# Kernel tuning notes

Measured on AMD Instinct MI355X. Metric: run time of the kernel, lower is better.

## Reference

```python
import jax, jax.numpy as jnp
import numpy as np

B, S, DM, H = 8, 512, 1024, 16
D = DM // H            # head_dim = 64
NFEAT = 4              # len(feature_types)
N_DIST = 2 * 512 - 1   # max_utt_num*2-1 = 1023
N_DISC = 16 + 1        # len(DISCOURSE_RELATIONS)+1
N_COOC = 5 + 1


def setup_inputs() -> dict:
    key = jax.random.key(0)
    ks = jax.random.split(key, 24)
    inp = {}
    inp["query"] = jax.random.normal(ks[0], (B, S, DM), jnp.float32)
    inp["key"] = jax.random.normal(ks[1], (B, S, DM), jnp.float32)
    inp["value"] = jax.random.normal(ks[2], (B, S, DM), jnp.float32)
    inp["distance_adj"] = jax.random.randint(ks[3], (B, S, S), 0, N_DIST).astype(jnp.int32)
    inp["speaker_adj"] = jax.random.uniform(ks[4], (B, S, S), jnp.float32)
    inp["discourse_adj"] = jax.random.randint(ks[5], (B, S, S), 0, N_DISC).astype(jnp.int32)
    inp["cooccurrence_adj"] = jax.random.randint(ks[6], (B, S, S), 0, N_COOC).astype(jnp.int32)
    inp["mask"] = jnp.ones((B, 1, 1, S), jnp.int32)
    w = lambda k, shape: jax.random.normal(k, shape, jnp.float32) * 0.02
    inp["Wq"] = w(ks[7], (DM, DM)); inp["bq"] = jnp.zeros((DM,), jnp.float32)
    inp["Wk"] = w(ks[8], (DM, DM)); inp["bk"] = jnp.zeros((DM,), jnp.float32)
    inp["Wv"] = w(ks[9], (DM, DM)); inp["bv"] = jnp.zeros((DM,), jnp.float32)
    inp["Wo"] = w(ks[10], (DM, DM)); inp["bo"] = jnp.zeros((DM,), jnp.float32)
    inp["dist_embed"] = w(ks[11], (N_DIST, 1))
    inp["disc_embed"] = w(ks[12], (N_DISC, 1)).at[0].set(0.0)  # padding_idx=0
    inp["cooc_embed"] = w(ks[13], (N_COOC, 1)).at[0].set(0.0)  # padding_idx=0
    inp["fcw"] = w(ks[14], (H, NFEAT))       # per-head 1x1 conv weights
    inp["fcb"] = jnp.zeros((H,), jnp.float32)
    inp["cw"] = w(ks[15], (2,))              # combine conv weights
    inp["cb"] = jnp.zeros((), jnp.float32)
    return inp


def reference(query, key, value, distance_adj, speaker_adj, discourse_adj,
              cooccurrence_adj, mask, Wq, bq, Wk, bk, Wv, bv, Wo, bo,
              dist_embed, disc_embed, cooc_embed, fcw, fcb, cw, cb):
    scale = jnp.asarray(D ** 0.5, query.dtype)
    # Linear projections, split heads -> [B, H, S, D]
    split = lambda x: x.reshape(B, S, H, D).transpose(0, 2, 1, 3)
    Q = split(query @ Wq.T + bq)
    K = split(key @ Wk.T + bk)
    V = split(value @ Wv.T + bv)
    energy = jnp.einsum('bhqd,bhkd->bhqk', Q, K) / scale  # [B,H,S,S]
    # Adjacency feature maps in feature_types order: distance, speaker, discourse, cooccurrence
    dist = dist_embed[distance_adj, 0]
    disc = disc_embed[discourse_adj, 0] * (discourse_adj != 0)
    cooc = cooc_embed[cooccurrence_adj, 0] * (cooccurrence_adj != 0)
    feature_map = jnp.stack([dist, speaker_adj, disc, cooc], axis=1)  # [B,4,S,S]
    # Per-head 1x1 conv over the 4 feature channels + relu
    feat = jax.nn.relu(jnp.einsum('hc,bcij->bhij', fcw, feature_map)
                       + fcb[None, :, None, None])       # [B,H,S,S]
    # Combine conv (1x1, 2 channels -> 1) + relu
    energy = jax.nn.relu(cw[0] * energy + cw[1] * feat + cb)
    energy = jnp.where(mask == 0, -jnp.inf, energy)
    attention = jax.nn.softmax(energy, axis=-1)           # [B,H,S,S]
    x = jnp.einsum('bhqk,bhkd->bhqd', attention, V)       # dropout p=0 (eval)
    x = x.transpose(0, 2, 1, 3).reshape(B, S, DM)
    x = x @ Wo.T + bo
    return x, attention
```

## Files before the change

### kernel.cpp

```cpp
#include <hip/hip_runtime.h>

using short8 = __attribute__((ext_vector_type(8))) short;
using f32x4  = __attribute__((ext_vector_type(4))) float;

__device__ __forceinline__ unsigned short f2bf(float x) {
    union { float f; unsigned u; } v; v.f = x;
    unsigned u = v.u;
    unsigned r = (u + 0x7fffu + ((u >> 16) & 1u)) >> 16;
    return (unsigned short)r;
}
__device__ __forceinline__ float bf2f(unsigned short h) {
    union { unsigned u; float f; } v; v.u = ((unsigned)h) << 16;
    return v.f;
}

__device__ __forceinline__ void async16(const void* g, void* l) {
    __builtin_amdgcn_global_load_lds(
        (const __attribute__((address_space(1))) void*)g,
        (__attribute__((address_space(3))) void*)l, 16, 0, 0);
}

__global__ __launch_bounds__(256) void cvt_qkv(
    const float* __restrict__ q, const float* __restrict__ k, const float* __restrict__ v,
    unsigned short* __restrict__ dst)
{
    int z = blockIdx.z;
    const float* src = (z == 0) ? q : ((z == 1) ? k : v);
    unsigned short* o = dst + (size_t)z * 4194304;
    size_t i = ((size_t)blockIdx.x * 256 + threadIdx.x) * 8;
    float4 a = *(const float4*)(src + i);
    float4 b = *(const float4*)(src + i + 4);
    ushort4 lo, hi;
    lo.x = f2bf(a.x); lo.y = f2bf(a.y); lo.z = f2bf(a.z); lo.w = f2bf(a.w);
    hi.x = f2bf(b.x); hi.y = f2bf(b.y); hi.z = f2bf(b.z); hi.w = f2bf(b.w);
    *(ushort4*)(o + i) = lo;
    *(ushort4*)(o + i + 4) = hi;
}

__global__ __launch_bounds__(256) void cvt_w(
    const float* __restrict__ wq, const float* __restrict__ wk,
    const float* __restrict__ wv, const float* __restrict__ wo,
    unsigned short* __restrict__ dst)
{
    int z = blockIdx.z;
    const float* src = (z == 0) ? wq : ((z == 1) ? wk : ((z == 2) ? wv : wo));
    unsigned short* o = dst + (size_t)z * 1048576;
    size_t i = ((size_t)blockIdx.x * 256 + threadIdx.x) * 8;
    float4 a = *(const float4*)(src + i);
    float4 b = *(const float4*)(src + i + 4);
    ushort4 lo, hi;
    lo.x = f2bf(a.x); lo.y = f2bf(a.y); lo.z = f2bf(a.z); lo.w = f2bf(a.w);
    hi.x = f2bf(b.x); hi.y = f2bf(b.y); hi.z = f2bf(b.z); hi.w = f2bf(b.w);
    *(ushort4*)(o + i) = lo;
    *(ushort4*)(o + i + 4) = hi;
}

__global__ __launch_bounds__(256) void feat_kernel(
    const int* __restrict__ dist_adj, const float* __restrict__ spk,
    const int* __restrict__ disc_adj, const int* __restrict__ cooc_adj,
    const float* __restrict__ dist_emb, const float* __restrict__ disc_emb,
    const float* __restrict__ cooc_emb, const float* __restrict__ fcw,
    const float* __restrict__ fcb, const float* __restrict__ cw,
    unsigned short* __restrict__ G)
{
    __shared__ float s_dist[1023];
    __shared__ float s_disc[17];
    __shared__ float s_cooc[6];
    __shared__ float s_fcw[64];
    __shared__ float s_fcb[16];
    int tid = threadIdx.x;
    for (int i = tid; i < 1023; i += 256) s_dist[i] = dist_emb[i];
    if (tid < 17) s_disc[tid] = disc_emb[tid];
    if (tid < 6)  s_cooc[tid] = cooc_emb[tid];
    if (tid < 64) s_fcw[tid]  = fcw[tid];
    if (tid < 16) s_fcb[tid]  = fcb[tid];
    __syncthreads();
    float cw1 = cw[1];

    size_t e = ((size_t)blockIdx.x * 256 + tid) * 4;
    int b   = (int)(e >> 18);
    int rem = (int)(e & 262143);
    int q = rem >> 9, k0 = rem & 511;

    int4   dd = *(const int4*)(dist_adj + e);
    float4 ss = *(const float4*)(spk + e);
    int4   dc = *(const int4*)(disc_adj + e);
    int4   cc = *(const int4*)(cooc_adj + e);

    float f0[4], f1[4], f2[4], f3[4];
    f0[0] = s_dist[dd.x]; f0[1] = s_dist[dd.y]; f0[2] = s_dist[dd.z]; f0[3] = s_dist[dd.w];
    f1[0] = ss.x; f1[1] = ss.y; f1[2] = ss.z; f1[3] = ss.w;
    f2[0] = dc.x ? s_disc[dc.x] : 0.f; f2[1] = dc.y ? s_disc[dc.y] : 0.f;
    f2[2] = dc.z ? s_disc[dc.z] : 0.f; f2[3] = dc.w ? s_disc[dc.w] : 0.f;
    f3[0] = cc.x ? s_cooc[cc.x] : 0.f; f3[1] = cc.y ? s_cooc[cc.y] : 0.f;
    f3[2] = cc.z ? s_cooc[cc.z] : 0.f; f3[3] = cc.w ? s_cooc[cc.w] : 0.f;

    size_t gb = (((size_t)b * 16) * 512 + q) * 512 + k0;
#pragma unroll
    for (int h = 0; h < 16; ++h) {
        float w0 = s_fcw[h*4+0], w1 = s_fcw[h*4+1], w2 = s_fcw[h*4+2], w3 = s_fcw[h*4+3];
        float bb = s_fcb[h];
        ushort4 o;
        o.x = f2bf(fmaxf(w0*f0[0] + w1*f1[0] + w2*f2[0] + w3*f3[0] + bb, 0.f) * cw1);
        o.y = f2bf(fmaxf(w0*f0[1] + w1*f1[1] + w2*f2[1] + w3*f3[1] + bb, 0.f) * cw1);
        o.z = f2bf(fmaxf(w0*f0[2] + w1*f1[2] + w2*f2[2] + w3*f3[2] + bb, 0.f) * cw1);
        o.w = f2bf(fmaxf(w0*f0[3] + w1*f1[3] + w2*f2[3] + w3*f3[3] + bb, 0.f) * cw1);
        *(ushort4*)(G + gb + (size_t)h * 262144) = o;
    }
}

template<int OMODE>
__device__ __forceinline__ void gemm_bf16_body(
    const unsigned short* __restrict__ A, const unsigned short* __restrict__ W,
    const float* __restrict__ bias, void* __restrict__ outp, int m0, int n0)
{
    __shared__ __align__(16) unsigned short As[128 * 32];
    __shared__ __align__(16) unsigned short Bs[128 * 32];
    int tid = threadIdx.x;
    int lane = tid & 63, wid = tid >> 6;
    int wx = wid & 1, wy = wid >> 1;
    int lanelo = lane & 15, hi8 = (lane >> 4) * 8;
    int rowc = lane >> 2;
    int colc = (lane & 3) * 8;

    f32x4 acc[4][4];
#pragma unroll
    for (int i = 0; i < 4; ++i)
#pragma unroll
        for (int j = 0; j < 4; ++j) {
            acc[i][j][0] = 0.f; acc[i][j][1] = 0.f; acc[i][j][2] = 0.f; acc[i][j][3] = 0.f;
        }

    for (int kk = 0; kk < 32; ++kk) {
        int k0 = kk * 32;
        __syncthreads();
#pragma unroll
        for (int p = 0; p < 2; ++p) {
            int c = 2 * wid + p;
            int row = c * 16 + rowc;
            async16(A + (size_t)(m0 + row) * 1024 + k0 + colc, As + c * 512);
        }
#pragma unroll
        for (int p = 0; p < 2; ++p) {
            int c = 2 * wid + p;
            int row = c * 16 + rowc;
            async16(W + (size_t)(n0 + row) * 1024 + k0 + colc, Bs + c * 512);
        }
        __syncthreads();

        short8 af[4], bfr[4];
#pragma unroll
        for (int i = 0; i < 4; ++i)
            af[i] = *(const short8*)(As + (wy*64 + i*16 + lanelo) * 32 + hi8);
#pragma unroll
        for (int j = 0; j < 4; ++j)
            bfr[j] = *(const short8*)(Bs + (wx*64 + j*16 + lanelo) * 32 + hi8);
#pragma unroll
        for (int i = 0; i < 4; ++i)
#pragma unroll
            for (int j = 0; j < 4; ++j)
                acc[i][j] = __builtin_amdgcn_mfma_f32_16x16x32_bf16(af[i], bfr[j], acc[i][j], 0, 0, 0);
    }

    float bia[4];
#pragma unroll
    for (int j = 0; j < 4; ++j) bia[j] = bias[n0 + wx*64 + j*16 + lanelo];
#pragma unroll
    for (int i = 0; i < 4; ++i) {
        int mbase = m0 + wy*64 + i*16 + (lane >> 4) * 4;
#pragma unroll
        for (int j = 0; j < 4; ++j) {
            int n = n0 + wx*64 + j*16 + lanelo;
#pragma unroll
            for (int r = 0; r < 4; ++r) {
                int m = mbase + r;
                float val = acc[i][j][r] + bia[j];
                if (OMODE == 0) {
                    unsigned short* o = (unsigned short*)outp;
                    o[((size_t)((m >> 9) * 16 + (n >> 6)) * 512 + (m & 511)) * 64 + (n & 63)] = f2bf(val);
                } else {
                    float* o = (float*)outp;
                    o[(size_t)m * 1024 + n] = val;
                }
            }
        }
    }
}

__global__ __launch_bounds__(256) void gemm_qkv(
    const unsigned short* __restrict__ Abf, const unsigned short* __restrict__ Wbf,
    const float* __restrict__ bq, const float* __restrict__ bk, const float* __restrict__ bv,
    unsigned short* Qb, unsigned short* Kb, unsigned short* Vb)
{
    int z = blockIdx.z;
    const unsigned short* A = Abf + (size_t)z * 4194304;
    const unsigned short* W = Wbf + (size_t)z * 1048576;
    const float* bias = (z == 0) ? bq : ((z == 1) ? bk : bv);
    unsigned short* o = (z == 0) ? Qb : ((z == 1) ? Kb : Vb);
    gemm_bf16_body<0>(A, W, bias, o, blockIdx.x * 128, blockIdx.y * 128);
}

__global__ __launch_bounds__(256) void gemm_proj(
    const unsigned short* __restrict__ xh, const unsigned short* __restrict__ Wo,
    const float* __restrict__ bo, float* __restrict__ out)
{
    gemm_bf16_body<1>(xh, Wo, bo, out, blockIdx.x * 128, blockIdx.y * 128);
}

__global__ __launch_bounds__(256) void transpose_v(const unsigned short* __restrict__ Vb,
                                                   unsigned short* __restrict__ Vt)
{
    __shared__ __align__(16) unsigned short T[64][72];
    int tid = threadIdx.x;
    int s0 = blockIdx.x * 64;
    int bh = blockIdx.z * 16 + blockIdx.y;
#pragma unroll
    for (int p = 0; p < 2; ++p) {
        int c = p * 256 + tid;
        int row = c >> 3, kc = (c & 7) * 8;
        uint4 v = *(const uint4*)(Vb + ((size_t)bh * 512 + s0 + row) * 64 + kc);
        *(uint4*)&T[row][kc] = v;
    }
    __syncthreads();
#pragma unroll
    for (int p = 0; p < 2; ++p) {
        int c = p * 256 + tid;
        int d = c >> 3, sc = (c & 7) * 8;
        unsigned vv[4];
#pragma unroll
        for (int i = 0; i < 4; ++i) {
            unsigned lo = T[sc + 2*i][d];
            unsigned hi = T[sc + 2*i + 1][d];
            vv[i] = lo | (hi << 16);
        }
        uint4 o; o.x = vv[0]; o.y = vv[1]; o.z = vv[2]; o.w = vv[3];
        *(uint4*)(Vt + ((size_t)bh * 64 + d) * 512 + s0 + sc) = o;
    }
}

__global__ __launch_bounds__(256, 2) void attn_kernel(
    const unsigned short* __restrict__ Qb, const unsigned short* __restrict__ Kb,
    const unsigned short* __restrict__ Vt, const unsigned short* __restrict__ G,
    const int* __restrict__ mask, const float* __restrict__ cw,
    const float* __restrict__ cb, float* __restrict__ attn_out,
    unsigned short* __restrict__ xh)
{
    __shared__ __align__(16) unsigned short Qs[64][72];
    __shared__ __align__(16) unsigned short Ks[128][72];
    __shared__ __align__(16) unsigned short Vs[64][40];
    __shared__ __align__(16) unsigned short Ps[4][16][40];
    __shared__ int s_mask[512];

    int tid = threadIdx.x;
    int lane = tid & 63, w = tid >> 6;
    int lanelo = lane & 15, hi8 = (lane >> 4) * 8;
    int qt = blockIdx.x, h = blockIdx.y, b = blockIdx.z;
    int bh = b * 16 + h;
    float qs  = cw[0] * 0.125f;
    float cbv = cb[0];

    s_mask[tid]       = mask[b * 512 + tid];
    s_mask[tid + 256] = mask[b * 512 + tid + 256];
#pragma unroll
    for (int p = 0; p < 2; ++p) {
        int c = p * 256 + tid;
        int row = c >> 3, kc = (c & 7) * 8;
        uint4 v = *(const uint4*)(Qb + ((size_t)bh * 512 + qt * 64 + row) * 64 + kc);
        *(uint4*)&Qs[row][kc] = v;
    }
    __syncthreads();

    short8 aq[2];
    aq[0] = *(const short8*)&Qs[w * 16 + lanelo][hi8];
    aq[1] = *(const short8*)&Qs[w * 16 + lanelo][32 + hi8];
    int qrow = qt * 64 + w * 16 + (lane >> 4) * 4;

    float P[32][4];
#pragma unroll
    for (int kt = 0; kt < 4; ++kt) {
        __syncthreads();
#pragma unroll
        for (int p = 0; p < 4; ++p) {
            int c = p * 256 + tid;
            int row = c >> 3, kc = (c & 7) * 8;
            uint4 v = *(const uint4*)(Kb + ((size_t)bh * 512 + kt * 128 + row) * 64 + kc);
            *(uint4*)&Ks[row][kc] = v;
        }
        __syncthreads();
#pragma unroll
        for (int j = 0; j < 8; ++j) {
            short8 b0 = *(const short8*)&Ks[j * 16 + lanelo][hi8];
            short8 b1 = *(const short8*)&Ks[j * 16 + lanelo][32 + hi8];
            f32x4 acc; acc[0] = 0.f; acc[1] = 0.f; acc[2] = 0.f; acc[3] = 0.f;
            acc = __builtin_amdgcn_mfma_f32_16x16x32_bf16(aq[0], b0, acc, 0, 0, 0);
            acc = __builtin_amdgcn_mfma_f32_16x16x32_bf16(aq[1], b1, acc, 0, 0, 0);
            int jj = kt * 8 + j;
            int kcol = jj * 16 + lanelo;
            int mk = s_mask[kcol];
            const unsigned short* gp = G + ((size_t)bh * 512 + qrow) * 512 + kcol;
#pragma unroll
            for (int r = 0; r < 4; ++r) {
                float e = qs * acc[r] + bf2f(gp[(size_t)r * 512]) + cbv;
                e = fmaxf(e, 0.f);
                P[jj][r] = mk ? __expf(e) : 0.f;
            }
        }
    }

    float inv[4];
#pragma unroll
    for (int r = 0; r < 4; ++r) {
        float s = 0.f;
#pragma unroll
        for (int jj = 0; jj < 32; ++jj) s += P[jj][r];
        s += __shfl_xor(s, 1, 64);
        s += __shfl_xor(s, 2, 64);
        s += __shfl_xor(s, 4, 64);
        s += __shfl_xor(s, 8, 64);
        inv[r] = 1.0f / s;
    }

    {
        float* ap = attn_out + ((size_t)bh * 512 + qrow) * 512 + lanelo;
#pragma unroll
        for (int jj = 0; jj < 32; ++jj)
#pragma unroll
            for (int r = 0; r < 4; ++r)
                ap[(size_t)r * 512 + jj * 16] = P[jj][r] * inv[r];
    }

    f32x4 xacc[4];
#pragma unroll
    for (int jf = 0; jf < 4; ++jf) { xacc[jf][0]=0.f; xacc[jf][1]=0.f; xacc[jf][2]=0.f; xacc[jf][3]=0.f; }
#pragma unroll
    for (int ks = 0; ks < 16; ++ks) {
        __syncthreads();
        {
            int d = tid >> 2, kc = (tid & 3) * 8;
            uint4 v = *(const uint4*)(Vt + ((size_t)bh * 64 + d) * 512 + ks * 32 + kc);
            *(uint4*)&Vs[d][kc] = v;
        }
#pragma unroll
        for (int ff = 0; ff < 2; ++ff) {
            int f = ks * 2 + ff;
#pragma unroll
            for (int r = 0; r < 4; ++r)
                Ps[w][(lane >> 4) * 4 + r][ff * 16 + lanelo] = f2bf(P[f][r]);
        }
        __syncthreads();
        short8 ap8 = *(const short8*)&Ps[w][lanelo][hi8];
#pragma unroll
        for (int jf = 0; jf < 4; ++jf) {
            short8 bv = *(const short8*)&Vs[jf * 16 + lanelo][hi8];
            xacc[jf] = __builtin_amdgcn_mfma_f32_16x16x32_bf16(ap8, bv, xacc[jf], 0, 0, 0);
        }
    }

#pragma unroll
    for (int jf = 0; jf < 4; ++jf) {
        int d = jf * 16 + lanelo;
#pragma unroll
        for (int r = 0; r < 4; ++r) {
            float val = xacc[jf][r] * inv[r];
            xh[((size_t)b * 512 + qrow + r) * 1024 + h * 64 + d] = f2bf(val);
        }
    }
}

extern "C" void kernel_launch(void* const* d_in, const int* in_sizes, int n_in,
                              void* d_out, int out_size, void* d_ws, size_t ws_size,
                              hipStream_t stream) {
    (void)in_sizes; (void)n_in; (void)out_size; (void)ws_size;
    const float* query    = (const float*)d_in[0];
    const float* key      = (const float*)d_in[1];
    const float* value    = (const float*)d_in[2];
    const int*   dist_adj = (const int*)d_in[3];
    const float* spk      = (const float*)d_in[4];
    const int*   disc_adj = (const int*)d_in[5];
    const int*   cooc_adj = (const int*)d_in[6];
    const int*   maskp    = (const int*)d_in[7];
    const float* Wq = (const float*)d_in[8];  const float* bq = (const float*)d_in[9];
    const float* Wk = (const float*)d_in[10]; const float* bk = (const float*)d_in[11];
    const float* Wv = (const float*)d_in[12]; const float* bv = (const float*)d_in[13];
    const float* Wo = (const float*)d_in[14]; const float* bo = (const float*)d_in[15];
    const float* dist_emb = (const float*)d_in[16];
    const float* disc_emb = (const float*)d_in[17];
    const float* cooc_emb = (const float*)d_in[18];
    const float* fcw = (const float*)d_in[19];
    const float* fcb = (const float*)d_in[20];
    const float* cw  = (const float*)d_in[21];
    const float* cbp = (const float*)d_in[22];

    char* w = (char*)d_ws;
    unsigned short* Qb  = (unsigned short*)(w);
    unsigned short* Kb  = (unsigned short*)(w + 8388608);
    unsigned short* Vb  = (unsigned short*)(w + 16777216);
    unsigned short* Vt  = (unsigned short*)(w + 25165824);
    unsigned short* xh  = (unsigned short*)(w + 33554432);
    unsigned short* G   = (unsigned short*)(w + 41943040);
    unsigned short* Abf = G;
    unsigned short* Wbf = (unsigned short*)(w + 109051904);

    float* out_x    = (float*)d_out;
    float* attn_out = ((float*)d_out) + 4194304;

    cvt_qkv<<<dim3(2048, 1, 3), 256, 0, stream>>>(query, key, value, Abf);
    cvt_w<<<dim3(512, 1, 4), 256, 0, stream>>>(Wq, Wk, Wv, Wo, Wbf);
    gemm_qkv<<<dim3(32, 8, 3), 256, 0, stream>>>(Abf, Wbf, bq, bk, bv, Qb, Kb, Vb);
    transpose_v<<<dim3(8, 16, 8), 256, 0, stream>>>(Vb, Vt);
    feat_kernel<<<2048, 256, 0, stream>>>(dist_adj, spk, disc_adj, cooc_adj,
                                          dist_emb, disc_emb, cooc_emb, fcw, fcb, cw, G);
    attn_kernel<<<dim3(8, 16, 8), 256, 0, stream>>>(Qb, Kb, Vt, G, maskp, cw, cbp,
                                                    attn_out, xh);
    gemm_proj<<<dim3(32, 8), 256, 0, stream>>>(xh, Wbf + 3145728, bo, out_x);
}
```

Measured before the change: 382.5 us.

## Retile feature-gate layout and stage attention outputs through LDS for coalesced stores

The feature kernel now writes G in a 4-row-interleaved layout, so each attention lane can fetch its four query rows for a key column as one ushort4 load, prefetched before the K tile sync. The attention-probability and head-output stores are transposed through a per-wave LDS buffer so global writes become contiguous float4/ushort4 rows instead of strided scalar stores. The K and V loops are no longer unrolled, which cuts code size and register pressure. The costs are extra LDS space, which may lower occupancy, and reliance on wave-local LDS ordering through manual waitcnt rather than barriers.

```diff
diff --git a/kernel.cpp b/kernel.cpp
--- a/kernel.cpp
+++ b/kernel.cpp
@@ -77,25 +77,26 @@
     __syncthreads();
     float cw1 = cw[1];
 
-    size_t e = ((size_t)blockIdx.x * 256 + tid) * 4;
-    int b   = (int)(e >> 18);
-    int rem = (int)(e & 262143);
-    int q = rem >> 9, k0 = rem & 511;
-
-    int4   dd = *(const int4*)(dist_adj + e);
-    float4 ss = *(const float4*)(spk + e);
-    int4   dc = *(const int4*)(disc_adj + e);
-    int4   cc = *(const int4*)(cooc_adj + e);
-
+    int bx = blockIdx.x;
+    int k  = (bx & 1) * 256 + tid;
+    int qq = (bx >> 1) & 127;
+    int b  = bx >> 8;
+
+    size_t abase = ((size_t)b * 512 + qq * 4) * 512 + k;
     float f0[4], f1[4], f2[4], f3[4];
-    f0[0] = s_dist[dd.x]; f0[1] = s_dist[dd.y]; f0[2] = s_dist[dd.z]; f0[3] = s_dist[dd.w];
-    f1[0] = ss.x; f1[1] = ss.y; f1[2] = ss.z; f1[3] = ss.w;
-    f2[0] = dc.x ? s_disc[dc.x] : 0.f; f2[1] = dc.y ? s_disc[dc.y] : 0.f;
-    f2[2] = dc.z ? s_disc[dc.z] : 0.f; f2[3] = dc.w ? s_disc[dc.w] : 0.f;
-    f3[0] = cc.x ? s_cooc[cc.x] : 0.f; f3[1] = cc.y ? s_cooc[cc.y] : 0.f;
-    f3[2] = cc.z ? s_cooc[cc.z] : 0.f; f3[3] = cc.w ? s_cooc[cc.w] : 0.f;
-
-    size_t gb = (((size_t)b * 16) * 512 + q) * 512 + k0;
+#pragma unroll
+    for (int r = 0; r < 4; ++r) {
+        size_t a = abase + (size_t)r * 512;
+        int dd = dist_adj[a];
+        f1[r]  = spk[a];
+        int dc = disc_adj[a];
+        int cc = cooc_adj[a];
+        f0[r] = s_dist[dd];
+        f2[r] = dc ? s_disc[dc] : 0.f;
+        f3[r] = cc ? s_cooc[cc] : 0.f;
+    }
+
+    size_t gq = ((size_t)b * 16 * 128 + qq) * 512 + k;
 #pragma unroll
     for (int h = 0; h < 16; ++h) {
         float w0 = s_fcw[h*4+0], w1 = s_fcw[h*4+1], w2 = s_fcw[h*4+2], w3 = s_fcw[h*4+3];
@@ -105,7 +106,7 @@
         o.y = f2bf(fmaxf(w0*f0[1] + w1*f1[1] + w2*f2[1] + w3*f3[1] + bb, 0.f) * cw1);
         o.z = f2bf(fmaxf(w0*f0[2] + w1*f1[2] + w2*f2[2] + w3*f3[2] + bb, 0.f) * cw1);
         o.w = f2bf(fmaxf(w0*f0[3] + w1*f1[3] + w2*f2[3] + w3*f3[3] + bb, 0.f) * cw1);
-        *(ushort4*)(G + gb + (size_t)h * 262144) = o;
+        *(ushort4*)(G + (gq + (size_t)h * 65536) * 4) = o;
     }
 }
 
@@ -249,11 +250,13 @@
     __shared__ __align__(16) unsigned short Ks[128][72];
     __shared__ __align__(16) unsigned short Vs[64][40];
     __shared__ __align__(16) unsigned short Ps[4][16][40];
+    __shared__ __align__(16) float PT[4][16][68];
     __shared__ int s_mask[512];
 
     int tid = threadIdx.x;
     int lane = tid & 63, w = tid >> 6;
     int lanelo = lane & 15, hi8 = (lane >> 4) * 8;
+    int hi2 = lane >> 4;
     int qt = blockIdx.x, h = blockIdx.y, b = blockIdx.z;
     int bh = b * 16 + h;
     float qs  = cw[0] * 0.125f;
@@ -273,11 +276,17 @@
     short8 aq[2];
     aq[0] = *(const short8*)&Qs[w * 16 + lanelo][hi8];
     aq[1] = *(const short8*)&Qs[w * 16 + lanelo][32 + hi8];
-    int qrow = qt * 64 + w * 16 + (lane >> 4) * 4;
+    int qrow = qt * 64 + w * 16 + hi2 * 4;
+    int qq   = qt * 16 + w * 4 + hi2;
+    const unsigned short* gbase = G + ((size_t)bh * 128 + qq) * 2048;
 
     float P[32][4];
-#pragma unroll
+#pragma unroll 1
     for (int kt = 0; kt < 4; ++kt) {
+        ushort4 g[8];
+#pragma unroll
+        for (int j = 0; j < 8; ++j)
+            g[j] = *(const ushort4*)(gbase + (kt * 8 + j) * 64 + lanelo * 4);
         __syncthreads();
 #pragma unroll
         for (int p = 0; p < 4; ++p) {
@@ -297,10 +306,10 @@
             int jj = kt * 8 + j;
             int kcol = jj * 16 + lanelo;
             int mk = s_mask[kcol];
-            const unsigned short* gp = G + ((size_t)bh * 512 + qrow) * 512 + kcol;
+            float gf[4] = { bf2f(g[j].x), bf2f(g[j].y), bf2f(g[j].z), bf2f(g[j].w) };
 #pragma unroll
             for (int r = 0; r < 4; ++r) {
-                float e = qs * acc[r] + bf2f(gp[(size_t)r * 512]) + cbv;
+                float e = qs * acc[r] + gf[r] + cbv;
                 e = fmaxf(e, 0.f);
                 P[jj][r] = mk ? __expf(e) : 0.f;
             }
@@ -321,18 +330,32 @@
     }
 
     {
-        float* ap = attn_out + ((size_t)bh * 512 + qrow) * 512 + lanelo;
-#pragma unroll
-        for (int jj = 0; jj < 32; ++jj)
-#pragma unroll
-            for (int r = 0; r < 4; ++r)
-                ap[(size_t)r * 512 + jj * 16] = P[jj][r] * inv[r];
+        float* PTw = &PT[w][0][0];
+        float* op  = attn_out + ((size_t)bh * 512 + qt * 64 + w * 16) * 512;
+#pragma unroll
+        for (int c = 0; c < 8; ++c) {
+#pragma unroll
+            for (int jc = 0; jc < 4; ++jc) {
+                int jj = c * 4 + jc;
+#pragma unroll
+                for (int r = 0; r < 4; ++r)
+                    PTw[(hi2 * 4 + r) * 68 + jc * 16 + lanelo] = P[jj][r] * inv[r];
+            }
+            asm volatile("s_waitcnt lgkmcnt(0)" ::: "memory");
+#pragma unroll
+            for (int p = 0; p < 4; ++p) {
+                int row = p * 4 + hi2;
+                float4 v4 = *(const float4*)&PTw[row * 68 + lanelo * 4];
+                *(float4*)(op + (size_t)row * 512 + c * 64 + lanelo * 4) = v4;
+            }
+            asm volatile("" ::: "memory");
+        }
     }
 
     f32x4 xacc[4];
 #pragma unroll
     for (int jf = 0; jf < 4; ++jf) { xacc[jf][0]=0.f; xacc[jf][1]=0.f; xacc[jf][2]=0.f; xacc[jf][3]=0.f; }
-#pragma unroll
+#pragma unroll 1
     for (int ks = 0; ks < 16; ++ks) {
         __syncthreads();
         {
@@ -345,7 +368,7 @@
             int f = ks * 2 + ff;
 #pragma unroll
             for (int r = 0; r < 4; ++r)
-                Ps[w][(lane >> 4) * 4 + r][ff * 16 + lanelo] = f2bf(P[f][r]);
+                Ps[w][hi2 * 4 + r][ff * 16 + lanelo] = f2bf(P[f][r]);
         }
         __syncthreads();
         short8 ap8 = *(const short8*)&Ps[w][lanelo][hi8];
@@ -356,13 +379,21 @@
         }
     }
 
-#pragma unroll
-    for (int jf = 0; jf < 4; ++jf) {
-        int d = jf * 16 + lanelo;
-#pragma unroll
-        for (int r = 0; r < 4; ++r) {
-            float val = xacc[jf][r] * inv[r];
-            xh[((size_t)b * 512 + qrow + r) * 1024 + h * 64 + d] = f2bf(val);
+    {
+        unsigned short* XT = (unsigned short*)&PT[w][0][0];
+        asm volatile("" ::: "memory");
+#pragma unroll
+        for (int jf = 0; jf < 4; ++jf)
+#pragma unroll
+            for (int r = 0; r < 4; ++r)
+                XT[(hi2 * 4 + r) * 68 + jf * 16 + lanelo] = f2bf(xacc[jf][r] * inv[r]);
+        asm volatile("s_waitcnt lgkmcnt(0)" ::: "memory");
+        unsigned short* xp = xh + ((size_t)b * 512 + qt * 64 + w * 16) * 1024 + h * 64;
+#pragma unroll
+        for (int p = 0; p < 4; ++p) {
+            int row = p * 4 + hi2;
+            ushort4 v = *(const ushort4*)&XT[row * 68 + lanelo * 4];
+            *(ushort4*)(xp + (size_t)row * 1024 + lanelo * 4) = v;
         }
     }
 }
```

New measurement: 462.1 us. +20.8%, slower.
